# Kernel tuning notes

Hardware: AMD Instinct MI355X
Metric: run time of the kernel (lower is better)

Reference implementation:

```python
import jax, jax.numpy as jnp
import numpy as np

# Dimensions
B = 8        # batch
T = 2048     # subtokens per sample
G = 1024     # pooled tokens (nodes + edges) per sample
NN = 600     # node slots per sample (seg_ids > 0)
NE = 424     # edge slots per sample (seg_ids < 0); NN + NE == G
D = 1024     # d_model == pretrained_dim (BART-large), so need_proj is False
V = 53587    # AMRBART vocab size
L = 2        # graph_layer_configs.nlayers


def setup_inputs() -> dict:
    key = jax.random.key(0)
    ks = jax.random.split(key, 8)
    scale = 0.02
    tokens_ids = jax.random.randint(ks[0], (B, T), 0, V, dtype=jnp.int32)
    # ragged token_splits encoded as segment ids; uniform groups of size T//G == 2
    token_group_ids = jnp.broadcast_to(
        jnp.arange(T, dtype=jnp.int32) // (T // G), (B, T))
    # seg_ids: +1 for node slots, -1 for edge slots (nodes-first layout, no pad)
    seg_ids = jnp.broadcast_to(
        jnp.concatenate([jnp.ones(NN, jnp.int32), -jnp.ones(NE, jnp.int32)]),
        (B, G))
    # torch-geometric style global edge index over batch-concatenated nodes
    src = jax.random.randint(ks[1], (B, NE), 0, NN, dtype=jnp.int32)
    dst = jax.random.randint(ks[2], (B, NE), 0, NN, dtype=jnp.int32)
    offs = (jnp.arange(B, dtype=jnp.int32) * NN)[:, None]
    edge_index = jnp.stack([(src + offs).reshape(-1), (dst + offs).reshape(-1)], 0)
    embedding_table = jax.random.normal(ks[3], (V, D), dtype=jnp.float32) * scale
    W_msg = jax.random.normal(ks[4], (L, D, D), dtype=jnp.float32) * scale
    W_upd = jax.random.normal(ks[5], (L, D, D), dtype=jnp.float32) * scale
    W_edge = jax.random.normal(ks[6], (L, D, D), dtype=jnp.float32) * scale
    return {"tokens_ids": tokens_ids, "token_group_ids": token_group_ids,
            "seg_ids": seg_ids, "edge_index": edge_index,
            "embedding_table": embedding_table,
            "W_msg": W_msg, "W_upd": W_upd, "W_edge": W_edge}


def reference(tokens_ids, token_group_ids, seg_ids, edge_index,
              embedding_table, W_msg, W_upd, W_edge):
    # 1) embedding lookup: [B, T, D]
    token_feats = embedding_table[tokens_ids]
    # 2) ragged subtoken mean-pool (torch.split + mean) via segment_sum
    seg_sum = jax.vmap(lambda x, ids: jax.ops.segment_sum(x, ids, num_segments=G))
    sums = seg_sum(token_feats, token_group_ids)                       # [B, G, D]
    counts = seg_sum(jnp.ones((B, T, 1), token_feats.dtype), token_group_ids)
    pooled = sums / jnp.maximum(counts, 1.0)                           # [B, G, D]
    # 3) gather node/edge feats (seg_ids layout is nodes-first, statically known)
    nodes = pooled[:, :NN].reshape(B * NN, D)
    edges = pooled[:, NN:].reshape(B * NE, D)
    src, dst = edge_index[0], edge_index[1]
    # 4) graph layers: edge-conditioned message passing with residuals
    for l in range(L):
        msg = jax.nn.relu((nodes[src] + edges) @ W_msg[l])             # [B*NE, D]
        agg = jax.ops.segment_sum(msg, dst, num_segments=B * NN)       # [B*NN, D]
        new_edges = edges + (nodes[src] + nodes[dst]) @ W_edge[l]
        nodes = nodes + agg @ W_upd[l]
        edges = new_edges
    # 5) scatter back into padded [B, G, D] tensor (boolean-mask scatter in torch)
    all_feats = jnp.concatenate(
        [nodes.reshape(B, NN, D), edges.reshape(B, NE, D)], axis=1)
    return all_feats
```

## Files before the change

### kernel.cpp

```cpp
#include <hip/hip_runtime.h>

constexpr int kB  = 8;
constexpr int kT  = 2048;
constexpr int kG  = 1024;
constexpr int kNN = 600;
constexpr int kNE = 424;
constexpr int kD  = 1024;
constexpr int kL  = 2;
constexpr int kBNN = kB * kNN;
constexpr int kBNE = kB * kNE;
static_assert(kBNE % 64 == 0, "M tiles exact");

typedef __attribute__((ext_vector_type(4))) float f32x4;
typedef __attribute__((ext_vector_type(8))) short bf16x8;
typedef __attribute__((address_space(1))) const void gas_t;
typedef __attribute__((address_space(3))) void las_t;

__device__ __forceinline__ unsigned short f2bf(float x) {
    union { float f; unsigned u; } v; v.f = x;
    unsigned r = v.u + 0x7FFF + ((v.u >> 16) & 1);
    return (unsigned short)(r >> 16);
}

__device__ __forceinline__ void glds16(const void* g, void* l) {
    __builtin_amdgcn_global_load_lds((gas_t*)g, (las_t*)l, 16, 0, 0);
}

__device__ __forceinline__ size_t edge_out_off(int row) {
    int b = row / kNE, r = row - b * kNE;
    return ((size_t)(b * kG + kNN + r)) * kD;
}
__device__ __forceinline__ size_t node_out_off(int n) {
    int b = n / kNN, g = n - b * kNN;
    return ((size_t)(b * kG + g)) * kD;
}

__global__ void bounds_kernel(const int* __restrict__ gid,
                              int* __restrict__ start, int* __restrict__ endp) {
    int idx = blockIdx.x * 256 + threadIdx.x;
    if (idx >= kB * kT) return;
    int b = idx / kT, t = idx - b * kT;
    int id = gid[idx];
    if (t == 0 || gid[idx - 1] != id) start[b * kG + id] = t;
    if (t == kT - 1 || gid[idx + 1] != id) endp[b * kG + id] = t + 1;
}

__global__ void pool_kernel(const int* __restrict__ tokens,
                            const int* __restrict__ start,
                            const int* __restrict__ endp,
                            const float* __restrict__ emb,
                            float* __restrict__ nodes,
                            float* __restrict__ edges) {
    int bg = blockIdx.x;
    int b = bg >> 10, g = bg & (kG - 1);
    int d = threadIdx.x * 4;
    int s = start[bg], e = endp[bg];
    float4 acc = make_float4(0.f, 0.f, 0.f, 0.f);
    for (int t = s; t < e; ++t) {
        int tok = tokens[b * kT + t];
        const float4 v = *(const float4*)(emb + (size_t)tok * kD + d);
        acc.x += v.x; acc.y += v.y; acc.z += v.z; acc.w += v.w;
    }
    int c = e - s;
    float sc = 1.0f / (float)(c > 0 ? c : 1);
    acc.x *= sc; acc.y *= sc; acc.z *= sc; acc.w *= sc;
    float* dstp = (g < kNN)
        ? (nodes + (size_t)(b * kNN + g) * kD + d)
        : (edges + (size_t)(b * kNE + (g - kNN)) * kD + d);
    *(float4*)dstp = acc;
}

__global__ __launch_bounds__(256) void wtrans_kernel(const float* __restrict__ Wm,
                                                     const float* __restrict__ Wu,
                                                     const float* __restrict__ We,
                                                     unsigned short* __restrict__ Wt) {
    int z = blockIdx.z;
    const float* W = (z < 2) ? (Wm + (size_t)z * kD * kD)
                   : (z < 4) ? (Wu + (size_t)(z - 2) * kD * kD)
                             : (We + (size_t)(z - 4) * kD * kD);
    unsigned short* out = Wt + (size_t)z * kD * kD;
    __shared__ float t[32][33];
    int n0 = blockIdx.x * 32, k0 = blockIdx.y * 32;
    int r = threadIdx.x >> 3, c4 = (threadIdx.x & 7) * 4;
    const float4 v = *(const float4*)(W + (size_t)(k0 + r) * kD + n0 + c4);
    t[r][c4] = v.x; t[r][c4 + 1] = v.y; t[r][c4 + 2] = v.z; t[r][c4 + 3] = v.w;
    __syncthreads();
    ushort4 o;
    o.x = f2bf(t[c4 + 0][r]); o.y = f2bf(t[c4 + 1][r]);
    o.z = f2bf(t[c4 + 2][r]); o.w = f2bf(t[c4 + 3][r]);
    *(ushort4*)(out + (size_t)(n0 + r) * kD + k0 + c4) = o;
}

template <int COPY>
__global__ void gather_kernel(const float* __restrict__ nodes,
                              const float* __restrict__ edges,
                              const int* __restrict__ src,
                              const int* __restrict__ dst,
                              unsigned short* __restrict__ bufM,
                              unsigned short* __restrict__ bufE,
                              float* __restrict__ out) {
    int d = threadIdx.x * 4;
    int e = blockIdx.x;
    if (COPY && e >= kBNE) {
        int n = e - kBNE;
        *(float4*)(out + node_out_off(n) + d) =
            *(const float4*)(nodes + (size_t)n * kD + d);
        return;
    }
    int s = src[e], t = dst[e];
    const float4 a = *(const float4*)(nodes + (size_t)s * kD + d);
    const float4 b = *(const float4*)(edges + (size_t)e * kD + d);
    const float4 c = *(const float4*)(nodes + (size_t)t * kD + d);
    ushort4 om, oe;
    om.x = f2bf(a.x + b.x); om.y = f2bf(a.y + b.y);
    om.z = f2bf(a.z + b.z); om.w = f2bf(a.w + b.w);
    oe.x = f2bf(a.x + c.x); oe.y = f2bf(a.y + c.y);
    oe.z = f2bf(a.z + c.z); oe.w = f2bf(a.w + c.w);
    *(ushort4*)(bufM + (size_t)e * kD + d) = om;
    *(ushort4*)(bufE + (size_t)e * kD + d) = oe;
}

template <int MODE>
__device__ __forceinline__ void gemm_body(const unsigned short* __restrict__ A,
                                          const unsigned short* __restrict__ Wt,
                                          float* __restrict__ Cf,
                                          unsigned short* __restrict__ Cb,
                                          const float* __restrict__ Ef,
                                          const int* __restrict__ idxp,
                                          char* smem, int bn, int bm) {
    const int tid = threadIdx.x;
    const int lane = tid & 63;
    const int w = tid >> 6;
    const int wr = w >> 1, wc = w & 1;
    const int row0 = bm * 64, col0 = bn * 128;

    const unsigned short* agp = A + (size_t)(row0 + (tid >> 2)) * kD + (tid & 3) * 8;
    const unsigned short* bgp0 = Wt + (size_t)(col0 + (tid >> 2)) * kD + (tid & 3) * 8;
    const unsigned short* bgp1 = Wt + (size_t)(col0 + 64 + (tid >> 2)) * kD + (tid & 3) * 8;
    const int woff = w * 1024;
    auto stage = [&](int bsel, int k0) {
        char* base = smem + bsel * 12288 + woff;
        glds16(agp + k0, base);
        glds16(bgp0 + k0, base + 4096);
        glds16(bgp1 + k0, base + 8192);
    };

    constexpr int nt = kD / 32;
    stage(0, 0);

    f32x4 acc[2][4] = {};
    const int l15 = lane & 15, kg = lane >> 4;
    for (int t = 0; t < nt; ++t) {
        char* bufc = smem + (t & 1) * 12288;
        __syncthreads();
        if (t + 1 < nt) stage((t + 1) & 1, (t + 1) * 32);
        bf16x8 af[2], bf[4];
#pragma unroll
        for (int i = 0; i < 2; ++i)
            af[i] = *(const bf16x8*)(bufc + ((wr * 32 + i * 16 + l15) * 32 + kg * 8) * 2);
#pragma unroll
        for (int j = 0; j < 4; ++j)
            bf[j] = *(const bf16x8*)(bufc + 4096 + ((wc * 64 + j * 16 + l15) * 32 + kg * 8) * 2);
#pragma unroll
        for (int i = 0; i < 2; ++i)
#pragma unroll
            for (int j = 0; j < 4; ++j)
                acc[i][j] = __builtin_amdgcn_mfma_f32_16x16x32_bf16(af[i], bf[j], acc[i][j], 0, 0, 0);
    }
    const int lr = (lane >> 4) * 4;
#pragma unroll
    for (int i = 0; i < 2; ++i) {
        int rbase = row0 + wr * 32 + i * 16 + lr;
#pragma unroll
        for (int r = 0; r < 4; ++r) {
            int row = rbase + r;
            if (MODE == 0) {
                unsigned short* cp = Cb + (size_t)row * kD;
#pragma unroll
                for (int j = 0; j < 4; ++j) {
                    int col = col0 + wc * 64 + j * 16 + l15;
                    cp[col] = f2bf(fmaxf(acc[i][j][r], 0.f));
                }
            } else if (MODE == 1) {
                float* cp = Cf + (size_t)row * kD;
#pragma unroll
                for (int j = 0; j < 4; ++j) {
                    int col = col0 + wc * 64 + j * 16 + l15;
                    cp[col] += acc[i][j][r];
                }
            } else if (MODE == 2) {
                const float* ep = Ef + (size_t)row * kD;
                float* op = Cf + edge_out_off(row);
#pragma unroll
                for (int j = 0; j < 4; ++j) {
                    int col = col0 + wc * 64 + j * 16 + l15;
                    op[col] = ep[col] + acc[i][j][r];
                }
            } else if (MODE == 3) {
                float* cp = Cf + (size_t)idxp[row] * kD;
#pragma unroll
                for (int j = 0; j < 4; ++j) {
                    int col = col0 + wc * 64 + j * 16 + l15;
                    atomicAdd(cp + col, acc[i][j][r]);
                }
            } else {
                float* cp = Cf + node_out_off(idxp[row]);
#pragma unroll
                for (int j = 0; j < 4; ++j) {
                    int col = col0 + wc * 64 + j * 16 + l15;
                    atomicAdd(cp + col, acc[i][j][r]);
                }
            }
        }
    }
}

__global__ __launch_bounds__(256) void gemm_dual_l0(const unsigned short* __restrict__ A0,
                                                    const unsigned short* __restrict__ B0,
                                                    unsigned short* __restrict__ C0,
                                                    const unsigned short* __restrict__ A1,
                                                    const unsigned short* __restrict__ B1,
                                                    float* __restrict__ C1) {
    __shared__ char smem[24576];
    if (blockIdx.z == 0)
        gemm_body<0>(A0, B0, nullptr, C0, nullptr, nullptr, smem, blockIdx.x, blockIdx.y);
    else
        gemm_body<1>(A1, B1, C1, nullptr, nullptr, nullptr, smem, blockIdx.x, blockIdx.y);
}

__global__ __launch_bounds__(256) void gemm_dual_l1(const unsigned short* __restrict__ A0,
                                                    const unsigned short* __restrict__ B0,
                                                    unsigned short* __restrict__ C0,
                                                    const unsigned short* __restrict__ A1,
                                                    const unsigned short* __restrict__ B1,
                                                    float* __restrict__ outp,
                                                    const float* __restrict__ edges) {
    __shared__ char smem[24576];
    if (blockIdx.z == 0)
        gemm_body<0>(A0, B0, nullptr, C0, nullptr, nullptr, smem, blockIdx.x, blockIdx.y);
    else
        gemm_body<2>(A1, B1, outp, nullptr, edges, nullptr, smem, blockIdx.x, blockIdx.y);
}

__global__ __launch_bounds__(256) void gemm_upd_l0(const unsigned short* __restrict__ A,
                                                   const unsigned short* __restrict__ B,
                                                   float* __restrict__ C,
                                                   const int* __restrict__ dstIdx) {
    __shared__ char smem[24576];
    gemm_body<3>(A, B, C, nullptr, nullptr, dstIdx, smem, blockIdx.x, blockIdx.y);
}

__global__ __launch_bounds__(256) void gemm_upd_l1(const unsigned short* __restrict__ A,
                                                   const unsigned short* __restrict__ B,
                                                   float* __restrict__ outp,
                                                   const int* __restrict__ dstIdx) {
    __shared__ char smem[24576];
    gemm_body<4>(A, B, outp, nullptr, nullptr, dstIdx, smem, blockIdx.x, blockIdx.y);
}

extern "C" void kernel_launch(void* const* d_in, const int* in_sizes, int n_in,
                              void* d_out, int out_size, void* d_ws, size_t ws_size,
                              hipStream_t stream) {
    const int*   tokens = (const int*)d_in[0];
    const int*   gids   = (const int*)d_in[1];
    const int*   eidx   = (const int*)d_in[3];
    const float* emb    = (const float*)d_in[4];
    const float* Wm     = (const float*)d_in[5];
    const float* Wu     = (const float*)d_in[6];
    const float* We     = (const float*)d_in[7];
    float* out = (float*)d_out;

    constexpr size_t szNodes = (size_t)kBNN * kD * 4;
    constexpr size_t szEdges = (size_t)kBNE * kD * 4;
    constexpr size_t szBufM  = (size_t)kBNE * kD * 2;
    constexpr size_t szBufE  = (size_t)kBNE * kD * 2;
    constexpr size_t szMsgB  = (size_t)kBNE * kD * 2;
    constexpr size_t szWt    = (size_t)6 * kD * kD * 2;
    char* ws = (char*)d_ws;
    float*          nodes = (float*)ws;
    float*          edges = (float*)(ws + szNodes);
    unsigned short* bufM  = (unsigned short*)(ws + szNodes + szEdges);
    unsigned short* bufE  = (unsigned short*)(ws + szNodes + szEdges + szBufM);
    unsigned short* msgb  = (unsigned short*)(ws + szNodes + szEdges + szBufM + szBufE);
    unsigned short* Wt    = (unsigned short*)(ws + szNodes + szEdges + szBufM + szBufE + szMsgB);
    int* start = (int*)(ws + szNodes + szEdges + szBufM + szBufE + szMsgB + szWt);
    int* endp  = start + kB * kG;

    const int* srcIdx = eidx;
    const int* dstIdx = eidx + kBNE;
    unsigned short* WtM = Wt;
    unsigned short* WtU = Wt + (size_t)2 * kD * kD;
    unsigned short* WtE = Wt + (size_t)4 * kD * kD;

    hipMemsetAsync(start, 0, (size_t)2 * kB * kG * sizeof(int), stream);
    bounds_kernel<<<(kB * kT + 255) / 256, 256, 0, stream>>>(gids, start, endp);
    pool_kernel<<<kB * kG, 256, 0, stream>>>(tokens, start, endp, emb, nodes, edges);
    wtrans_kernel<<<dim3(kD / 32, kD / 32, 6), 256, 0, stream>>>(Wm, Wu, We, Wt);

    constexpr int mt = kBNE / 64;
    const dim3 gdual(kD / 128, mt, 2);
    const dim3 gupd(kD / 128, mt, 1);

    gather_kernel<0><<<kBNE, 256, 0, stream>>>(nodes, edges, srcIdx, dstIdx, bufM, bufE, out);
    gemm_dual_l0<<<gdual, 256, 0, stream>>>(bufM, WtM, msgb, bufE, WtE, edges);
    gemm_upd_l0<<<gupd, 256, 0, stream>>>(msgb, WtU, nodes, dstIdx);

    gather_kernel<1><<<kBNE + kBNN, 256, 0, stream>>>(nodes, edges, srcIdx, dstIdx, bufM, bufE, out);
    gemm_dual_l1<<<gdual, 256, 0, stream>>>(bufM, WtM + (size_t)kD * kD, msgb,
                                            bufE, WtE + (size_t)kD * kD, out, edges);
    gemm_upd_l1<<<gupd, 256, 0, stream>>>(msgb, WtU + (size_t)kD * kD, out, dstIdx);
}
```

Measured before the change: 173.9 us.

## Fuse prep kernels with binary-search bounds and deepen GEMM load pipeline

Replaces the memset, bounds, pool and weight-transpose launches with one prep kernel whose blocks either pool a group or transpose a weight tile. Segment bounds are found by binary search over the sorted group ids, so the bounds pass and its scratch arrays go away. The GEMM main loop now issues async LDS loads two stages ahead, using explicit vmcnt/lgkmcnt waits and two barriers per step, so global loads overlap more with MFMA work. The extra barrier and the binary search add some overhead, and the search assumes the group ids are sorted.

```diff
diff --git a/kernel.cpp b/kernel.cpp
--- a/kernel.cpp
+++ b/kernel.cpp
@@ -35,60 +35,57 @@
     return ((size_t)(b * kG + g)) * kD;
 }
 
-__global__ void bounds_kernel(const int* __restrict__ gid,
-                              int* __restrict__ start, int* __restrict__ endp) {
-    int idx = blockIdx.x * 256 + threadIdx.x;
-    if (idx >= kB * kT) return;
-    int b = idx / kT, t = idx - b * kT;
-    int id = gid[idx];
-    if (t == 0 || gid[idx - 1] != id) start[b * kG + id] = t;
-    if (t == kT - 1 || gid[idx + 1] != id) endp[b * kG + id] = t + 1;
-}
-
-__global__ void pool_kernel(const int* __restrict__ tokens,
-                            const int* __restrict__ start,
-                            const int* __restrict__ endp,
-                            const float* __restrict__ emb,
-                            float* __restrict__ nodes,
-                            float* __restrict__ edges) {
-    int bg = blockIdx.x;
-    int b = bg >> 10, g = bg & (kG - 1);
-    int d = threadIdx.x * 4;
-    int s = start[bg], e = endp[bg];
-    float4 acc = make_float4(0.f, 0.f, 0.f, 0.f);
-    for (int t = s; t < e; ++t) {
-        int tok = tokens[b * kT + t];
-        const float4 v = *(const float4*)(emb + (size_t)tok * kD + d);
-        acc.x += v.x; acc.y += v.y; acc.z += v.z; acc.w += v.w;
+__global__ __launch_bounds__(256) void prep_kernel(const int* __restrict__ tokens,
+                                                   const int* __restrict__ gids,
+                                                   const float* __restrict__ emb,
+                                                   float* __restrict__ nodes,
+                                                   float* __restrict__ edges,
+                                                   const float* __restrict__ Wm,
+                                                   const float* __restrict__ Wu,
+                                                   const float* __restrict__ We,
+                                                   unsigned short* __restrict__ Wt) {
+    __shared__ float tbuf[32][33];
+    int bx = blockIdx.x;
+    if (bx < kB * kG) {
+        int b = bx >> 10, g = bx & (kG - 1);
+        int d = threadIdx.x * 4;
+        const int* row = gids + (size_t)b * kT;
+        int lo = 0, hi = kT;
+        while (lo < hi) { int m = (lo + hi) >> 1; if (row[m] < g) lo = m + 1; else hi = m; }
+        int s = lo; hi = kT;
+        while (lo < hi) { int m = (lo + hi) >> 1; if (row[m] <= g) lo = m + 1; else hi = m; }
+        int e = lo;
+        float4 acc = make_float4(0.f, 0.f, 0.f, 0.f);
+        for (int t = s; t < e; ++t) {
+            int tok = tokens[(size_t)b * kT + t];
+            const float4 v = *(const float4*)(emb + (size_t)tok * kD + d);
+            acc.x += v.x; acc.y += v.y; acc.z += v.z; acc.w += v.w;
+        }
+        int c = e - s;
+        float sc = 1.0f / (float)(c > 0 ? c : 1);
+        acc.x *= sc; acc.y *= sc; acc.z *= sc; acc.w *= sc;
+        float* dstp = (g < kNN)
+            ? (nodes + (size_t)(b * kNN + g) * kD + d)
+            : (edges + (size_t)(b * kNE + (g - kNN)) * kD + d);
+        *(float4*)dstp = acc;
+    } else {
+        int idx = bx - kB * kG;
+        int z = idx >> 10;
+        int rem = idx & 1023;
+        int n0 = (rem & 31) * 32, k0 = (rem >> 5) * 32;
+        const float* W = (z < 2) ? (Wm + (size_t)z * kD * kD)
+                       : (z < 4) ? (Wu + (size_t)(z - 2) * kD * kD)
+                                 : (We + (size_t)(z - 4) * kD * kD);
+        unsigned short* outp = Wt + (size_t)z * kD * kD;
+        int r = threadIdx.x >> 3, c4 = (threadIdx.x & 7) * 4;
+        const float4 v = *(const float4*)(W + (size_t)(k0 + r) * kD + n0 + c4);
+        tbuf[r][c4] = v.x; tbuf[r][c4 + 1] = v.y; tbuf[r][c4 + 2] = v.z; tbuf[r][c4 + 3] = v.w;
+        __syncthreads();
+        ushort4 o;
+        o.x = f2bf(tbuf[c4 + 0][r]); o.y = f2bf(tbuf[c4 + 1][r]);
+        o.z = f2bf(tbuf[c4 + 2][r]); o.w = f2bf(tbuf[c4 + 3][r]);
+        *(ushort4*)(outp + (size_t)(n0 + r) * kD + k0 + c4) = o;
     }
-    int c = e - s;
-    float sc = 1.0f / (float)(c > 0 ? c : 1);
-    acc.x *= sc; acc.y *= sc; acc.z *= sc; acc.w *= sc;
-    float* dstp = (g < kNN)
-        ? (nodes + (size_t)(b * kNN + g) * kD + d)
-        : (edges + (size_t)(b * kNE + (g - kNN)) * kD + d);
-    *(float4*)dstp = acc;
-}
-
-__global__ __launch_bounds__(256) void wtrans_kernel(const float* __restrict__ Wm,
-                                                     const float* __restrict__ Wu,
-                                                     const float* __restrict__ We,
-                                                     unsigned short* __restrict__ Wt) {
-    int z = blockIdx.z;
-    const float* W = (z < 2) ? (Wm + (size_t)z * kD * kD)
-                   : (z < 4) ? (Wu + (size_t)(z - 2) * kD * kD)
-                             : (We + (size_t)(z - 4) * kD * kD);
-    unsigned short* out = Wt + (size_t)z * kD * kD;
-    __shared__ float t[32][33];
-    int n0 = blockIdx.x * 32, k0 = blockIdx.y * 32;
-    int r = threadIdx.x >> 3, c4 = (threadIdx.x & 7) * 4;
-    const float4 v = *(const float4*)(W + (size_t)(k0 + r) * kD + n0 + c4);
-    t[r][c4] = v.x; t[r][c4 + 1] = v.y; t[r][c4 + 2] = v.z; t[r][c4 + 3] = v.w;
-    __syncthreads();
-    ushort4 o;
-    o.x = f2bf(t[c4 + 0][r]); o.y = f2bf(t[c4 + 1][r]);
-    o.z = f2bf(t[c4 + 2][r]); o.w = f2bf(t[c4 + 3][r]);
-    *(ushort4*)(out + (size_t)(n0 + r) * kD + k0 + c4) = o;
 }
 
 template <int COPY>
@@ -147,13 +144,15 @@
 
     constexpr int nt = kD / 32;
     stage(0, 0);
+    stage(1, 32);
 
     f32x4 acc[2][4] = {};
     const int l15 = lane & 15, kg = lane >> 4;
     for (int t = 0; t < nt; ++t) {
         char* bufc = smem + (t & 1) * 12288;
-        __syncthreads();
-        if (t + 1 < nt) stage((t + 1) & 1, (t + 1) * 32);
+        if (t < nt - 1) asm volatile("s_waitcnt vmcnt(3)" ::: "memory");
+        else            asm volatile("s_waitcnt vmcnt(0)" ::: "memory");
+        __builtin_amdgcn_s_barrier();
         bf16x8 af[2], bf[4];
 #pragma unroll
         for (int i = 0; i < 2; ++i)
@@ -161,6 +160,9 @@
 #pragma unroll
         for (int j = 0; j < 4; ++j)
             bf[j] = *(const bf16x8*)(bufc + 4096 + ((wc * 64 + j * 16 + l15) * 32 + kg * 8) * 2);
+        asm volatile("s_waitcnt lgkmcnt(0)" ::: "memory");
+        __builtin_amdgcn_s_barrier();
+        if (t + 2 < nt) stage(t & 1, (t + 2) * 32);
 #pragma unroll
         for (int i = 0; i < 2; ++i)
 #pragma unroll
@@ -275,7 +277,6 @@
     constexpr size_t szBufM  = (size_t)kBNE * kD * 2;
     constexpr size_t szBufE  = (size_t)kBNE * kD * 2;
     constexpr size_t szMsgB  = (size_t)kBNE * kD * 2;
-    constexpr size_t szWt    = (size_t)6 * kD * kD * 2;
     char* ws = (char*)d_ws;
     float*          nodes = (float*)ws;
     float*          edges = (float*)(ws + szNodes);
@@ -283,8 +284,6 @@
     unsigned short* bufE  = (unsigned short*)(ws + szNodes + szEdges + szBufM);
     unsigned short* msgb  = (unsigned short*)(ws + szNodes + szEdges + szBufM + szBufE);
     unsigned short* Wt    = (unsigned short*)(ws + szNodes + szEdges + szBufM + szBufE + szMsgB);
-    int* start = (int*)(ws + szNodes + szEdges + szBufM + szBufE + szMsgB + szWt);
-    int* endp  = start + kB * kG;
 
     const int* srcIdx = eidx;
     const int* dstIdx = eidx + kBNE;
@@ -292,10 +291,8 @@
     unsigned short* WtU = Wt + (size_t)2 * kD * kD;
     unsigned short* WtE = Wt + (size_t)4 * kD * kD;
 
-    hipMemsetAsync(start, 0, (size_t)2 * kB * kG * sizeof(int), stream);
-    bounds_kernel<<<(kB * kT + 255) / 256, 256, 0, stream>>>(gids, start, endp);
-    pool_kernel<<<kB * kG, 256, 0, stream>>>(tokens, start, endp, emb, nodes, edges);
-    wtrans_kernel<<<dim3(kD / 32, kD / 32, 6), 256, 0, stream>>>(Wm, Wu, We, Wt);
+    prep_kernel<<<kB * kG + 6 * 1024, 256, 0, stream>>>(
+        tokens, gids, emb, nodes, edges, Wm, Wu, We, Wt);
 
     constexpr int mt = kBNE / 64;
     const dim3 gdual(kD / 128, mt, 2);
```

New measurement: 166.5 us. 4.3% less time.
